# Kernel optimization log

Measured on AMD Instinct MI355X. Metric: run time of the kernel, lower is better.

## Reference

```python
import jax, jax.numpy as jnp
import numpy as np

B, CIN, COUT, H, W, KH, KW, G = 16, 64, 128, 128, 128, 3, 3, 4


def setup_inputs() -> dict:
    key = jax.random.key(0)
    k1, k2, k3 = jax.random.split(key, 3)
    x = jax.random.normal(k1, (B, CIN, H, W), dtype=jnp.float32)
    spline_weights = jax.random.normal(k2, (COUT, CIN, KH, KW, G), dtype=jnp.float32)
    basis_weights = jax.random.normal(k3, (COUT, CIN, KH, KW), dtype=jnp.float32)
    return {"x": x, "spline_weights": spline_weights, "basis_weights": basis_weights}


def _conv_same(inp, w):
    # NCHW x OIHW -> NCHW, stride 1, SAME padding (pad = k//2, matches torch F.pad)
    return jax.lax.conv_general_dilated(
        inp, w, window_strides=(1, 1),
        padding=[(KH // 2, KH // 2), (KW // 2, KW // 2)],
        dimension_numbers=("NCHW", "OIHW", "NCHW"))


def reference(x, spline_weights, basis_weights):
    # spline branch: patch broadcast over grid then summed == conv with grid-summed kernel
    w_spline = spline_weights.sum(axis=-1)  # (COUT, CIN, KH, KW)
    # basis branch: silu applied to (zero-)padded patches; silu(0)=0 so equals conv(silu(x))
    return _conv_same(x, w_spline) + _conv_same(jax.nn.silu(x), basis_weights)
```

## Files before the change

### kernel.cpp

```cpp
#include <hip/hip_runtime.h>
#include <math.h>

#define B_    16
#define CIN   64
#define COUT  128
#define H_    128
#define W_    128
#define CI2   128
#define KTOT  1152

typedef __bf16 bf16x8 __attribute__((ext_vector_type(8)));
typedef float  f32x4  __attribute__((ext_vector_type(4)));

#define XT_BYTES  ((size_t)B_ * H_ * W_ * CI2 * 2)
#define WC_BYTES  ((size_t)COUT * KTOT * 2)
#define Z_OFF     (XT_BYTES + WC_BYTES)
#define WS_NEED   (Z_OFF + 4096)

__global__ __launch_bounds__(256) void w_prep(const float* __restrict__ sw,
                                              const float* __restrict__ bw,
                                              __bf16* __restrict__ wc,
                                              float* __restrict__ zp) {
    const int i = blockIdx.x * 256 + threadIdx.x;
    if (blockIdx.x == 0) zp[threadIdx.x] = 0.f;
    if (i >= COUT * KTOT) return;
    const int co = i / KTOT, k = i - co * KTOT;
    const int tap = k >> 7, ci2 = k & 127;
    float v;
    if (ci2 < CIN) {
        const float* p = sw + ((size_t)(co * CIN + ci2) * 9 + tap) * 4;
        v = p[0] + p[1] + p[2] + p[3];
    } else {
        v = bw[(size_t)(co * CIN + (ci2 - CIN)) * 9 + tap];
    }
    const int wm = co >> 6, m = (co >> 4) & 3, l15 = co & 15;
    const int ks = (k >> 5) & 3, lq = (k >> 3) & 3, e = k & 7;
    const size_t off =
        ((size_t)(tap * 32 + (wm * 4 + m) * 4 + ks) * 64 + lq * 16 + l15) * 8 + e;
    wc[off] = (__bf16)v;
}

__global__ __launch_bounds__(256) void xt_prep(const float* __restrict__ x,
                                               __bf16* __restrict__ xt) {
    __shared__ __align__(16) __bf16 tile[64][136];
    const int t  = threadIdx.x;
    const int w0 = blockIdx.x * 64;
    const int h  = blockIdx.y;
    const int b  = blockIdx.z;
    const float* xb = x + ((size_t)(b * CIN) * H_ + h) * W_ + w0;
#pragma unroll
    for (int rep = 0; rep < 16; ++rep) {
        const int idx = rep * 256 + t;
        const int ci = idx >> 6, w = idx & 63;
        const float v = xb[(size_t)ci * H_ * W_ + w];
        tile[w][ci]       = (__bf16)v;
        tile[w][CIN + ci] = (__bf16)(v / (1.f + __expf(-v)));
    }
    __syncthreads();
    __bf16* ob = xt + (((size_t)b * H_ + h) * W_ + w0) * CI2;
#pragma unroll
    for (int rep = 0; rep < 4; ++rep) {
        const int idx = rep * 256 + t;
        const int w = idx >> 4, sl = idx & 15;
        *(bf16x8*)(ob + (size_t)w * CI2 + sl * 8) = *(const bf16x8*)(&tile[w][sl * 8]);
    }
}

__global__ __launch_bounds__(256, 2) void kan_mfma(const __bf16* __restrict__ xt,
                                                   const __bf16* __restrict__ wc,
                                                   const float* __restrict__ zp,
                                                   float* __restrict__ out) {
    __shared__ __align__(16) char xs[2880 * 16];
    __shared__ __align__(16) char as_[2048 * 16];
    const int t    = threadIdx.x;
    const int lane = t & 63, wave = t >> 6;
    const int wm = wave >> 1, wn = wave & 1;
    const int l15 = lane & 15, lq = lane >> 4;

    const int orig = blockIdx.x;
    const int wid  = (orig & 7) * 256 + (orig >> 3);
    const int b  = wid >> 7;
    const int hy = (wid & 127) >> 3, wx = wid & 7;
    const int w0 = wx * 16, h0 = hy * 8;

    const size_t xbase = (size_t)b * (H_ * W_ * CI2);
#pragma unroll
    for (int i = 0; i < 12; ++i) {
        const int s = i * 256 + t;
        if (s < 2880) {
            const int pos = s >> 4, q = s & 15;
            const int ih = pos / 18, iw = pos - ih * 18;
            const int gh = h0 + ih - 1, gw = w0 + iw - 1;
            const int chunk = q ^ (pos & 15);
            const void* src;
            if (gh >= 0 && gh < H_ && gw >= 0 && gw < W_)
                src = (const void*)(xt + xbase + ((size_t)(gh * W_ + gw)) * CI2 + chunk * 8);
            else
                src = (const void*)zp;
            __builtin_amdgcn_global_load_lds(
                (const __attribute__((address_space(1))) unsigned int*)src,
                (__attribute__((address_space(3))) unsigned int*)(xs + s * 16), 16, 0, 0);
        }
    }

#define STAGEA_(tp)                                                             \
    _Pragma("unroll")                                                           \
    for (int i = 0; i < 8; ++i) {                                               \
        const int s = i * 256 + t;                                              \
        __builtin_amdgcn_global_load_lds(                                       \
            (const __attribute__((address_space(1))) unsigned int*)              \
                (wc + ((size_t)(tp) * 2048 + s) * 8),                           \
            (__attribute__((address_space(3))) unsigned int*)(as_ + s * 16),    \
            16, 0, 0);                                                          \
    }

    STAGEA_(0);
    __syncthreads();

    f32x4 acc[4][4] = {};
    int pos0[4];
#pragma unroll
    for (int n = 0; n < 4; ++n) pos0[n] = (wn * 4 + n) * 18 + l15;

#pragma unroll 1
    for (int tap = 0; tap < 9; ++tap) {
        const int kh = (tap * 11) >> 5;
        const int kw = tap - kh * 3;
        const int dpos = kh * 18 + kw;
#pragma unroll
        for (int ks = 0; ks < 4; ++ks) {
            bf16x8 af[4], bfr[4];
#pragma unroll
            for (int m = 0; m < 4; ++m)
                af[m] = *(const bf16x8*)(as_ + ((wm * 4 + m) * 4 + ks) * 1024 + lane * 16);
#pragma unroll
            for (int n = 0; n < 4; ++n) {
                const int pos_ = pos0[n] + dpos;
                const int swz_ = (ks * 4 + lq) ^ (pos_ & 15);
                bfr[n] = *(const bf16x8*)(xs + pos_ * 256 + swz_ * 16);
            }
#pragma unroll
            for (int m = 0; m < 4; ++m)
#pragma unroll
                for (int n = 0; n < 4; ++n)
                    acc[m][n] = __builtin_amdgcn_mfma_f32_16x16x32_bf16(
                        af[m], bfr[n], acc[m][n], 0, 0, 0);
        }
        if (tap < 8) {
            __syncthreads();
            STAGEA_(tap + 1);
            __syncthreads();
        }
    }

    float* ob = out + (size_t)b * COUT * H_ * W_;
#pragma unroll
    for (int m = 0; m < 4; ++m) {
        const int co = wm * 64 + m * 16 + lq * 4;
#pragma unroll
        for (int n = 0; n < 4; ++n) {
            const int ph = wn * 4 + n;
            float* p = ob + ((size_t)co * H_ + (h0 + ph)) * W_ + (w0 + l15);
#pragma unroll
            for (int r = 0; r < 4; ++r)
                p[(size_t)r * H_ * W_] = acc[m][n][r];
        }
    }
#undef STAGEA_
}

#define TS   16
#define COB  8
#define TIN  18
__global__ __launch_bounds__(256) void spline_sum_kernel(const float* __restrict__ sw,
                                                         float* __restrict__ wsum) {
    int i = blockIdx.x * 256 + threadIdx.x;
    if (i < COUT * CIN * 9) {
        const float4 v = *reinterpret_cast<const float4*>(sw + (size_t)i * 4);
        wsum[i] = v.x + v.y + v.z + v.w;
    }
}
__global__ __launch_bounds__(256) void kan_conv(const float* __restrict__ x,
                                                const float* __restrict__ wsp,
                                                const float* __restrict__ wb,
                                                float* __restrict__ out) {
    __shared__ float xsm[TIN][20];
    __shared__ float ssm[TIN][20];
    const int t = threadIdx.x, tx = t & 15, ty = t >> 4;
    const int w0 = (blockIdx.x & 7) * TS, h0 = (blockIdx.x >> 3) * TS;
    const int co0 = blockIdx.y * COB, b = blockIdx.z;
    float acc[COB];
#pragma unroll
    for (int i = 0; i < COB; ++i) acc[i] = 0.f;
    const float* xb = x + (size_t)b * CIN * H_ * W_;
    for (int ci = 0; ci < CIN; ++ci) {
        __syncthreads();
        const float* xc = xb + (size_t)ci * H_ * W_;
        for (int p = t; p < TIN * TIN; p += 256) {
            int r = p / TIN, c = p - r * TIN;
            int ih = h0 + r - 1, iw = w0 + c - 1;
            float v = 0.f;
            if (ih >= 0 && ih < H_ && iw >= 0 && iw < W_) v = xc[ih * W_ + iw];
            xsm[r][c] = v;
            ssm[r][c] = v / (1.f + expf(-v));
        }
        __syncthreads();
        float xv[9], sv[9];
#pragma unroll
        for (int kh = 0; kh < 3; ++kh)
#pragma unroll
            for (int kw = 0; kw < 3; ++kw) {
                xv[kh * 3 + kw] = xsm[ty + kh][tx + kw];
                sv[kh * 3 + kw] = ssm[ty + kh][tx + kw];
            }
#pragma unroll
        for (int co = 0; co < COB; ++co) {
            const float* w1 = wsp + ((size_t)(co0 + co) * CIN + ci) * 9;
            const float* w2 = wb  + ((size_t)(co0 + co) * CIN + ci) * 9;
#pragma unroll
            for (int k = 0; k < 9; ++k)
                acc[co] += xv[k] * w1[k] + sv[k] * w2[k];
        }
    }
    const int oh = h0 + ty, ow = w0 + tx;
#pragma unroll
    for (int co = 0; co < COB; ++co)
        out[(((size_t)b * COUT + (co0 + co)) * H_ + oh) * W_ + ow] = acc[co];
}

extern "C" void kernel_launch(void* const* d_in, const int* in_sizes, int n_in,
                              void* d_out, int out_size, void* d_ws, size_t ws_size,
                              hipStream_t stream) {
    const float* x  = (const float*)d_in[0];
    const float* sw = (const float*)d_in[1];
    const float* bw = (const float*)d_in[2];
    float* out = (float*)d_out;

    if (ws_size >= WS_NEED) {
        __bf16* xt = (__bf16*)d_ws;
        __bf16* wc = (__bf16*)((char*)d_ws + XT_BYTES);
        float*  zp = (float*)((char*)d_ws + Z_OFF);
        w_prep<<<(COUT * KTOT + 255) / 256, 256, 0, stream>>>(sw, bw, wc, zp);
        xt_prep<<<dim3(2, H_, B_), 256, 0, stream>>>(x, xt);
        kan_mfma<<<dim3(2048), 256, 0, stream>>>(xt, wc, zp, out);
    } else {
        float* wsum = (float*)d_ws;
        spline_sum_kernel<<<(COUT * CIN * 9 + 255) / 256, 256, 0, stream>>>(sw, wsum);
        kan_conv<<<dim3(64, COUT / COB, B_), 256, 0, stream>>>(x, wsum, bw, out);
    }
}
```

Before: 113.7 us.

## Double-buffer weight tiles in half-tap chunks to overlap loads with MFMA

Splits each tap's weight tile into two half-K chunks, ping-ponged between two LDS buffers, and reorders the packed weight layout to match. The next half-chunk is loaded with global_load_lds while MFMAs run on the current one, so each step needs one barrier instead of a stall-then-load pair. This hides the weight staging latency and keeps total LDS use the same. It relies on the async LDS loads being complete at the next barrier, and on the new packed layout matching the new indexing.

```diff
diff --git a/kernel.cpp b/kernel.cpp
--- a/kernel.cpp
+++ b/kernel.cpp
@@ -35,8 +35,9 @@
     }
     const int wm = co >> 6, m = (co >> 4) & 3, l15 = co & 15;
     const int ks = (k >> 5) & 3, lq = (k >> 3) & 3, e = k & 7;
-    const size_t off =
-        ((size_t)(tap * 32 + (wm * 4 + m) * 4 + ks) * 64 + lq * 16 + l15) * 8 + e;
+    const int hh = tap * 2 + (ks >> 1);
+    const int f  = (wm * 4 + m) * 2 + (ks & 1);
+    const size_t off = ((size_t)(hh * 16 + f)) * 512 + (lq * 16 + l15) * 8 + e;
     wc[off] = (__bf16)v;
 }
 
@@ -71,7 +72,8 @@
                                                    const float* __restrict__ zp,
                                                    float* __restrict__ out) {
     __shared__ __align__(16) char xs[2880 * 16];
-    __shared__ __align__(16) char as_[2048 * 16];
+    __shared__ __align__(16) char asA[1024 * 16];
+    __shared__ __align__(16) char asB[1024 * 16];
     const int t    = threadIdx.x;
     const int lane = t & 63, wave = t >> 6;
     const int wm = wave >> 1, wn = wave & 1;
@@ -103,18 +105,41 @@
         }
     }
 
-#define STAGEA_(tp)                                                             \
+#define STAGEH_(buf, hh)                                                        \
     _Pragma("unroll")                                                           \
-    for (int i = 0; i < 8; ++i) {                                               \
+    for (int i = 0; i < 4; ++i) {                                               \
         const int s = i * 256 + t;                                              \
         __builtin_amdgcn_global_load_lds(                                       \
             (const __attribute__((address_space(1))) unsigned int*)              \
-                (wc + ((size_t)(tp) * 2048 + s) * 8),                           \
-            (__attribute__((address_space(3))) unsigned int*)(as_ + s * 16),    \
+                (wc + (size_t)(hh) * 8192 + s * 8),                             \
+            (__attribute__((address_space(3))) unsigned int*)((buf) + s * 16),  \
             16, 0, 0);                                                          \
     }
 
-    STAGEA_(0);
+#define COMPUTE2_(buf, kss)                                                     \
+    _Pragma("unroll")                                                           \
+    for (int k2 = 0; k2 < 2; ++k2) {                                            \
+        const int ks = (kss) + k2;                                              \
+        bf16x8 af[4], bfr[4];                                                   \
+        _Pragma("unroll")                                                       \
+        for (int m = 0; m < 4; ++m)                                             \
+            af[m] = *(const bf16x8*)((buf) +                                    \
+                ((wm * 4 + m) * 2 + (ks & 1)) * 1024 + lane * 16);              \
+        _Pragma("unroll")                                                       \
+        for (int n = 0; n < 4; ++n) {                                           \
+            const int pos_ = pos0[n] + dpos;                                    \
+            const int swz_ = (ks * 4 + lq) ^ (pos_ & 15);                       \
+            bfr[n] = *(const bf16x8*)(xs + pos_ * 256 + swz_ * 16);             \
+        }                                                                       \
+        _Pragma("unroll")                                                       \
+        for (int m = 0; m < 4; ++m)                                             \
+            _Pragma("unroll")                                                   \
+            for (int n = 0; n < 4; ++n)                                         \
+                acc[m][n] = __builtin_amdgcn_mfma_f32_16x16x32_bf16(            \
+                    af[m], bfr[n], acc[m][n], 0, 0, 0);                         \
+    }
+
+    STAGEH_(asA, 0);
     __syncthreads();
 
     f32x4 acc[4][4] = {};
@@ -127,30 +152,14 @@
         const int kh = (tap * 11) >> 5;
         const int kw = tap - kh * 3;
         const int dpos = kh * 18 + kw;
-#pragma unroll
-        for (int ks = 0; ks < 4; ++ks) {
-            bf16x8 af[4], bfr[4];
-#pragma unroll
-            for (int m = 0; m < 4; ++m)
-                af[m] = *(const bf16x8*)(as_ + ((wm * 4 + m) * 4 + ks) * 1024 + lane * 16);
-#pragma unroll
-            for (int n = 0; n < 4; ++n) {
-                const int pos_ = pos0[n] + dpos;
-                const int swz_ = (ks * 4 + lq) ^ (pos_ & 15);
-                bfr[n] = *(const bf16x8*)(xs + pos_ * 256 + swz_ * 16);
-            }
-#pragma unroll
-            for (int m = 0; m < 4; ++m)
-#pragma unroll
-                for (int n = 0; n < 4; ++n)
-                    acc[m][n] = __builtin_amdgcn_mfma_f32_16x16x32_bf16(
-                        af[m], bfr[n], acc[m][n], 0, 0, 0);
-        }
-        if (tap < 8) {
-            __syncthreads();
-            STAGEA_(tap + 1);
-            __syncthreads();
-        }
+
+        STAGEH_(asB, tap * 2 + 1);
+        COMPUTE2_(asA, 0);
+        __syncthreads();
+
+        if (tap < 8) STAGEH_(asA, tap * 2 + 2);
+        COMPUTE2_(asB, 2);
+        __syncthreads();
     }
 
     float* ob = out + (size_t)b * COUT * H_ * W_;
@@ -166,7 +175,8 @@
                 p[(size_t)r * H_ * W_] = acc[m][n][r];
         }
     }
-#undef STAGEA_
+#undef STAGEH_
+#undef COMPUTE2_
 }
 
 #define TS   16
```

Result: no change. 114.7 us (+0.9%).
